# Kernel optimization log

Measured on AMD Instinct MI355X. Metric: run time of the kernel, lower is better.

Reference implementation:

```python
import jax, jax.numpy as jnp
import numpy as np

B, IN, OUT, LMAX = 20000, 128, 128, 6
M = (LMAX + 1) ** 2  # 49

def _make_expand_index(lmax):
    idx = np.zeros((lmax + 1) ** 2, dtype=np.int64)
    for l in range(lmax + 1):
        idx[l * l: l * l + 2 * l + 1] = l
    return jnp.asarray(idx)

def setup_inputs() -> dict:
    key = jax.random.key(0)
    k1, k2 = jax.random.split(key)
    bound = 1.0 / np.sqrt(IN)
    input_embedding = jax.random.normal(k1, (B, M, IN), dtype=jnp.float32)
    weight = jax.random.uniform(k2, (LMAX + 1, OUT, IN), dtype=jnp.float32,
                                minval=-bound, maxval=bound)
    bias = jnp.zeros((OUT,), dtype=jnp.float32)
    expand_index = _make_expand_index(LMAX)
    return {"input_embedding": input_embedding, "weight": weight,
            "bias": bias, "expand_index": expand_index}

def reference(input_embedding, weight, bias, expand_index):
    # gather per-degree weight to per-m weight: [M, out, in]
    w = weight[expand_index]
    # batched per-m matmul: [B, M, in] x [M, out, in] -> [B, M, out]
    out = jnp.einsum('bmi,moi->bmo', input_embedding, w)
    # bias applies only to the l=0 (m=0) row
    out = out.at[:, 0, :].add(bias)
    return out
```

## Files before the change

### kernel.cpp

```cpp
#include <hip/hip_runtime.h>

#define B_TOT   20000
#define M_TOT   49
#define IN_DIM  128
#define OUT_DIM 128
#define TILE_B  128

typedef short v8s __attribute__((ext_vector_type(8)));
typedef float v4f __attribute__((ext_vector_type(4)));

__device__ __forceinline__ short f2bf(float x) {
    union { float f; unsigned int u; } c; c.f = x;
    unsigned int r = c.u + 0x7FFFu + ((c.u >> 16) & 1u);
    return (short)(r >> 16);
}

__global__ void so3_linear_kernel(const float* __restrict__ inp,
                                  const float* __restrict__ wgt,
                                  const float* __restrict__ bias,
                                  float* __restrict__ out) {
    __shared__ __align__(16) short As[TILE_B][IN_DIM];
    __shared__ __align__(16) short Ws[OUT_DIM][IN_DIM];

    const int tid  = threadIdx.x;
    const int m    = blockIdx.y;
    const int b0   = blockIdx.x * TILE_B;

    int l = 0;
    while ((l + 1) * (l + 1) <= m) ++l;

    const float4* inp4 = (const float4*)inp;
    #pragma unroll
    for (int it = 0; it < 16; ++it) {
        int f  = it * 256 + tid;
        int r  = f >> 5;
        int c4 = f & 31;
        int gb = b0 + r;
        float4 v = make_float4(0.f, 0.f, 0.f, 0.f);
        if (gb < B_TOT)
            v = inp4[((size_t)gb * M_TOT + m) * (IN_DIM / 4) + c4];
        short4 s;
        s.x = f2bf(v.x); s.y = f2bf(v.y); s.z = f2bf(v.z); s.w = f2bf(v.w);
        int sc = (((c4 >> 1) ^ (r & 15)) << 3) + ((c4 & 1) << 2);
        *(short4*)&As[r][sc] = s;
    }

    const float4* wp4 = (const float4*)(wgt + (size_t)l * OUT_DIM * IN_DIM);
    #pragma unroll
    for (int it = 0; it < 16; ++it) {
        int f  = it * 256 + tid;
        int r  = f >> 5;
        int c4 = f & 31;
        float4 v = wp4[r * (IN_DIM / 4) + c4];
        short4 s;
        s.x = f2bf(v.x); s.y = f2bf(v.y); s.z = f2bf(v.z); s.w = f2bf(v.w);
        int sc = (((c4 >> 1) ^ (r & 15)) << 3) + ((c4 & 1) << 2);
        *(short4*)&Ws[r][sc] = s;
    }

    __syncthreads();

    const int wave = tid >> 6;
    const int lane = tid & 63;
    const int lr   = lane & 15;
    const int quad = lane >> 4;
    const int wrow = (wave >> 1) * 64;
    const int wcol = (wave & 1) * 64;

    v4f acc[4][4];
    #pragma unroll
    for (int i = 0; i < 4; ++i)
        #pragma unroll
        for (int j = 0; j < 4; ++j)
            acc[i][j] = (v4f)(0.f);

    #pragma unroll
    for (int kk = 0; kk < 4; ++kk) {
        const int chunk = kk * 4 + quad;
        const int sc    = ((chunk ^ lr) << 3);
        v8s af[4], bf[4];
        #pragma unroll
        for (int i = 0; i < 4; ++i)
            af[i] = *(const v8s*)&As[wrow + i * 16 + lr][sc];
        #pragma unroll
        for (int j = 0; j < 4; ++j)
            bf[j] = *(const v8s*)&Ws[wcol + j * 16 + lr][sc];
        #pragma unroll
        for (int i = 0; i < 4; ++i)
            #pragma unroll
            for (int j = 0; j < 4; ++j)
                acc[i][j] = __builtin_amdgcn_mfma_f32_16x16x32_bf16(
                                af[i], bf[j], acc[i][j], 0, 0, 0);
    }

    #pragma unroll
    for (int i = 0; i < 4; ++i) {
        const int rowbase = wrow + i * 16 + quad * 4;
        #pragma unroll
        for (int j = 0; j < 4; ++j) {
            const int col = wcol + j * 16 + lr;
            float bv = 0.f;
            if (m == 0) bv = bias[col];
            #pragma unroll
            for (int r = 0; r < 4; ++r) {
                const int gb = b0 + rowbase + r;
                if (gb < B_TOT) {
                    size_t off = ((size_t)gb * M_TOT + m) * OUT_DIM + col;
                    out[off] = acc[i][j][r] + bv;
                }
            }
        }
    }
}

extern "C" void kernel_launch(void* const* d_in, const int* in_sizes, int n_in,
                              void* d_out, int out_size, void* d_ws, size_t ws_size,
                              hipStream_t stream) {
    const float* inp  = (const float*)d_in[0];
    const float* wgt  = (const float*)d_in[1];
    const float* bias = (const float*)d_in[2];
    float* out = (float*)d_out;

    dim3 grid((B_TOT + TILE_B - 1) / TILE_B, M_TOT);
    dim3 block(256);
    so3_linear_kernel<<<grid, block, 0, stream>>>(inp, wgt, bias, out);
}
```

Baseline: 1.029 ms.

## Load input activations directly into MFMA registers and write float4 outputs

Drops the shared-memory staging of the input tile: each lane loads its own row segments from global memory straight into registers, converts them to bf16 per k-step, and prefetches the next k-chunk. The MFMA operands are swapped so the accumulator holds contiguous output columns per lane, which allows 16-byte vector stores instead of scalar stores. Launch bounds are added to target three blocks per CU, helped by the halved LDS footprint. The risks are more register pressure and less coalesced global reads (32-byte segments per lane across rows).

```diff
diff --git a/kernel.cpp b/kernel.cpp
--- a/kernel.cpp
+++ b/kernel.cpp
@@ -15,11 +15,11 @@
     return (short)(r >> 16);
 }
 
-__global__ void so3_linear_kernel(const float* __restrict__ inp,
-                                  const float* __restrict__ wgt,
-                                  const float* __restrict__ bias,
-                                  float* __restrict__ out) {
-    __shared__ __align__(16) short As[TILE_B][IN_DIM];
+__global__ __launch_bounds__(256, 3)
+void so3_linear_kernel(const float* __restrict__ inp,
+                       const float* __restrict__ wgt,
+                       const float* __restrict__ bias,
+                       float* __restrict__ out) {
     __shared__ __align__(16) short Ws[OUT_DIM][IN_DIM];
 
     const int tid  = threadIdx.x;
@@ -29,20 +29,26 @@
     int l = 0;
     while ((l + 1) * (l + 1) <= m) ++l;
 
-    const float4* inp4 = (const float4*)inp;
+    const int wave = tid >> 6;
+    const int lane = tid & 63;
+    const int lr   = lane & 15;
+    const int quad = lane >> 4;
+    const int wrow = (wave >> 1) * 64;
+    const int wcol = (wave & 1) * 64;
+
+    const float* arow[4];
     #pragma unroll
-    for (int it = 0; it < 16; ++it) {
-        int f  = it * 256 + tid;
-        int r  = f >> 5;
-        int c4 = f & 31;
-        int gb = b0 + r;
-        float4 v = make_float4(0.f, 0.f, 0.f, 0.f);
-        if (gb < B_TOT)
-            v = inp4[((size_t)gb * M_TOT + m) * (IN_DIM / 4) + c4];
-        short4 s;
-        s.x = f2bf(v.x); s.y = f2bf(v.y); s.z = f2bf(v.z); s.w = f2bf(v.w);
-        int sc = (((c4 >> 1) ^ (r & 15)) << 3) + ((c4 & 1) << 2);
-        *(short4*)&As[r][sc] = s;
+    for (int i = 0; i < 4; ++i) {
+        int gb = b0 + wrow + i * 16 + lr;
+        int gc = gb < B_TOT ? gb : B_TOT - 1;
+        arow[i] = inp + ((size_t)gc * M_TOT + m) * IN_DIM + quad * 8;
+    }
+
+    float4 pa[4][2];
+    #pragma unroll
+    for (int i = 0; i < 4; ++i) {
+        pa[i][0] = *(const float4*)(arow[i]);
+        pa[i][1] = *(const float4*)(arow[i] + 4);
     }
 
     const float4* wp4 = (const float4*)(wgt + (size_t)l * OUT_DIM * IN_DIM);
@@ -60,13 +66,6 @@
 
     __syncthreads();
 
-    const int wave = tid >> 6;
-    const int lane = tid & 63;
-    const int lr   = lane & 15;
-    const int quad = lane >> 4;
-    const int wrow = (wave >> 1) * 64;
-    const int wcol = (wave & 1) * 64;
-
     v4f acc[4][4];
     #pragma unroll
     for (int i = 0; i < 4; ++i)
@@ -76,12 +75,24 @@
 
     #pragma unroll
     for (int kk = 0; kk < 4; ++kk) {
+        v8s af[4];
+        #pragma unroll
+        for (int i = 0; i < 4; ++i) {
+            af[i][0] = f2bf(pa[i][0].x); af[i][1] = f2bf(pa[i][0].y);
+            af[i][2] = f2bf(pa[i][0].z); af[i][3] = f2bf(pa[i][0].w);
+            af[i][4] = f2bf(pa[i][1].x); af[i][5] = f2bf(pa[i][1].y);
+            af[i][6] = f2bf(pa[i][1].z); af[i][7] = f2bf(pa[i][1].w);
+        }
+        if (kk < 3) {
+            #pragma unroll
+            for (int i = 0; i < 4; ++i) {
+                pa[i][0] = *(const float4*)(arow[i] + (kk + 1) * 32);
+                pa[i][1] = *(const float4*)(arow[i] + (kk + 1) * 32 + 4);
+            }
+        }
         const int chunk = kk * 4 + quad;
         const int sc    = ((chunk ^ lr) << 3);
-        v8s af[4], bf[4];
-        #pragma unroll
-        for (int i = 0; i < 4; ++i)
-            af[i] = *(const v8s*)&As[wrow + i * 16 + lr][sc];
+        v8s bf[4];
         #pragma unroll
         for (int j = 0; j < 4; ++j)
             bf[j] = *(const v8s*)&Ws[wcol + j * 16 + lr][sc];
@@ -90,24 +101,25 @@
             #pragma unroll
             for (int j = 0; j < 4; ++j)
                 acc[i][j] = __builtin_amdgcn_mfma_f32_16x16x32_bf16(
-                                af[i], bf[j], acc[i][j], 0, 0, 0);
+                                bf[j], af[i], acc[i][j], 0, 0, 0);
     }
 
     #pragma unroll
     for (int i = 0; i < 4; ++i) {
-        const int rowbase = wrow + i * 16 + quad * 4;
-        #pragma unroll
-        for (int j = 0; j < 4; ++j) {
-            const int col = wcol + j * 16 + lr;
-            float bv = 0.f;
-            if (m == 0) bv = bias[col];
+        const int gb = b0 + wrow + i * 16 + lr;
+        if (gb < B_TOT) {
+            float* orow = out + ((size_t)gb * M_TOT + m) * OUT_DIM;
             #pragma unroll
-            for (int r = 0; r < 4; ++r) {
-                const int gb = b0 + rowbase + r;
-                if (gb < B_TOT) {
-                    size_t off = ((size_t)gb * M_TOT + m) * OUT_DIM + col;
-                    out[off] = acc[i][j][r] + bv;
+            for (int j = 0; j < 4; ++j) {
+                const int col = wcol + j * 16 + quad * 4;
+                v4f v = acc[i][j];
+                if (m == 0) {
+                    v[0] += bias[col];
+                    v[1] += bias[col + 1];
+                    v[2] += bias[col + 2];
+                    v[3] += bias[col + 3];
                 }
+                *(v4f*)(orow + col) = v;
             }
         }
     }
```

After: 884.5 us. 1.16x faster.
